# Performance work log

Measured on AMD Instinct MI355X. Metric: run time of the kernel, lower is better.

Reference implementation:

```python
import jax, jax.numpy as jnp
import numpy as np

B, S = 64, 4096
IN_CH, HID, OUT_CH, LIFT, MODES, NLAYERS = 2, 64, 3, 256, 16, 4
FREQ = S // 2 + 1


def setup_inputs() -> dict:
    key = jax.random.key(0)
    ks = jax.random.split(key, 10)
    g = lambda k, shp, s=0.02: (jax.random.normal(k, shp, jnp.float32) * s)
    return {
        "x": jax.random.normal(ks[0], (B, S, IN_CH), jnp.float32),
        "lift_w1": g(ks[1], (LIFT, IN_CH), 0.1),
        "lift_b1": jnp.zeros((LIFT,), jnp.float32),
        "lift_w2": g(ks[2], (HID, LIFT)),
        "lift_b2": jnp.zeros((HID,), jnp.float32),
        # spectral weights per layer: real/imag parts of [in, out, modes]
        "spec_wr": g(ks[3], (NLAYERS, HID, HID, MODES), 1.0 / HID),
        "spec_wi": g(ks[4], (NLAYERS, HID, HID, MODES), 1.0 / HID),
        "skip_w": g(ks[5], (NLAYERS, HID, HID)),
        "skip_b": jnp.zeros((NLAYERS, HID), jnp.float32),
        "proj_w1": g(ks[6], (LIFT, HID)),
        "proj_b1": jnp.zeros((LIFT,), jnp.float32),
        "proj_w2": g(ks[7], (OUT_CH, LIFT)),
        "proj_b2": jnp.zeros((OUT_CH,), jnp.float32),
    }


def _gelu(x):
    return jax.nn.gelu(x, approximate=False)  # torch F.gelu default (exact)


def reference(x, lift_w1, lift_b1, lift_w2, lift_b2, spec_wr, spec_wi,
              skip_w, skip_b, proj_w1, proj_b1, proj_w2, proj_b2):
    # x: (B, S, 2) -> permute to channels-first (B, 2, S), fused into einsum
    h = jnp.einsum('bsi,oi->bos', x, lift_w1) + lift_b1[None, :, None]  # (B, 256, S)
    h = _gelu(h)
    h = jnp.einsum('bcs,oc->bos', h, lift_w2) + lift_b2[None, :, None]  # (B, 64, S)

    for l in range(NLAYERS):
        # spectral conv: rfft -> keep low modes -> complex mix -> irfft
        xf = jnp.fft.rfft(h, axis=-1)[..., :MODES]            # (B, HID, MODES) complex
        w = spec_wr[l] + 1j * spec_wi[l]                       # (HID, HID, MODES)
        yk = jnp.einsum('bim,iom->bom', xf, w)                 # (B, HID, MODES)
        yf = jnp.zeros((h.shape[0], HID, FREQ), jnp.complex64).at[..., :MODES].set(yk)
        spec = jnp.fft.irfft(yf, n=S, axis=-1)                 # (B, HID, S)
        skip = jnp.einsum('bcs,oc->bos', h, skip_w[l]) + skip_b[l][None, :, None]
        h = spec + skip
        if l < NLAYERS - 1:
            h = _gelu(h)

    h = _gelu(jnp.einsum('bcs,oc->bos', h, proj_w1) + proj_b1[None, :, None])
    out_seq = jnp.einsum('bcs,oc->bos', h, proj_w2) + proj_b2[None, :, None]  # (B, 3, S)
    # AdaptiveAvgPool1d(1) + squeeze(-1) == mean over length
    return out_seq.mean(axis=-1)  # (B, 3)
```

## Files before the change

### kernel.cpp

```cpp
#include <hip/hip_runtime.h>
#include <math.h>

#define B_    64
#define S_    4096
#define HID   64
#define LIFT  256
#define MODES 16
#define NL    4

#define OFF_H     0
#define OFF_ETB   16777216
#define OFF_XFY   (OFF_ETB + 131072)
#define OFF_SKH   (OFF_XFY + 131072)
#define OFF_SKL   (OFF_SKH + 8192)
#define OFF_W2HI  (OFF_SKL + 8192)
#define OFF_W2LO  (OFF_W2HI + 8192)
#define OFF_P1HI  (OFF_W2LO + 8192)
#define OFF_P1LO  (OFF_P1HI + 8192)
#define OFF_PART  (OFF_P1LO + 8192)
#define OFF_W1B   (OFF_PART + 12288)

typedef short short8 __attribute__((ext_vector_type(8)));
typedef float f32x4  __attribute__((ext_vector_type(4)));
typedef unsigned uint8v __attribute__((ext_vector_type(8)));
#define MFMA16 __builtin_amdgcn_mfma_f32_16x16x32_bf16

__device__ __forceinline__ float gelu_f(float x) {
  float z = fabsf(x) * 0.70710678118654752440f;
  float p = 1.0f + z * (0.0705230784f + z * (0.0422820123f +
            z * (0.0092705272f + z * (0.0001520143f +
            z * (0.0002765672f + z * 0.0000430638f)))));
  float r = __builtin_amdgcn_rcpf(p);
  r = r * r;
  r = r * r;
  r = r * r;
  r = r * r;
  float q = 0.5f * r;
  float phi = (x >= 0.0f) ? (1.0f - q) : q;
  return x * phi;
}
__device__ __forceinline__ unsigned short f2bf(float x) {
  unsigned u = __float_as_uint(x);
  u += 0x7fffu + ((u >> 16) & 1u);
  return (unsigned short)(u >> 16);
}
__device__ __forceinline__ float bf2f(unsigned short b) {
  return __uint_as_float(((unsigned)b) << 16);
}
__device__ __forceinline__ unsigned packsplit(float x) {
  unsigned short hi = f2bf(x);
  unsigned short lo = f2bf(x - bf2f(hi));
  return (unsigned)hi | ((unsigned)lo << 16);
}
__device__ __forceinline__ void unpk8(const unsigned* pk, short8& h8, short8& l8) {
  #pragma unroll
  for (int j = 0; j < 8; ++j) {
    unsigned u = pk[j];
    h8[j] = (short)(u & 0xffffu);
    l8[j] = (short)(u >> 16);
  }
}

__global__ void k_init(const float* __restrict__ lift_w2,
                       const float* __restrict__ skip_w,
                       const float* __restrict__ proj_w1,
                       const float* __restrict__ lift_w1,
                       const float* __restrict__ lift_b1,
                       float* __restrict__ ws) {
  unsigned* etab = (unsigned*)(ws + OFF_ETB);
  unsigned short* skh = (unsigned short*)(ws + OFF_SKH);
  unsigned short* skl = (unsigned short*)(ws + OFF_SKL);
  unsigned short* w2hi = (unsigned short*)(ws + OFF_W2HI);
  unsigned short* w2lo = (unsigned short*)(ws + OFF_W2LO);
  unsigned short* p1hi = (unsigned short*)(ws + OFF_P1HI);
  unsigned short* p1lo = (unsigned short*)(ws + OFF_P1LO);
  float4* w1b = (float4*)(ws + OFF_W1B);
  int idx = blockIdx.x * 256 + threadIdx.x;
  int stride = gridDim.x * 256;
  for (int k = idx; k < 4096 * 32; k += stride) {
    int s = k >> 5, c = k & 31;
    int m = c & 15;
    int r = (m * s) & 4095;
    float th = (float)(2.0 * 3.14159265358979323846 / 4096.0) * (float)r;
    float sn, cn; sincosf(th, &sn, &cn);
    float v = (c < 16) ? cn : -sn;
    etab[k] = packsplit(v);
  }
  for (int k = idx; k < NL * HID * HID; k += stride) {
    float w = skip_w[k];
    unsigned short hi = f2bf(w);
    skh[k] = hi; skl[k] = f2bf(w - bf2f(hi));
  }
  for (int k = idx; k < HID * LIFT; k += stride) {
    float w = lift_w2[k];
    unsigned short hi = f2bf(w);
    w2hi[k] = hi; w2lo[k] = f2bf(w - bf2f(hi));
  }
  for (int k = idx; k < LIFT * HID; k += stride) {
    float w = proj_w1[k];
    unsigned short hi = f2bf(w);
    p1hi[k] = hi; p1lo[k] = f2bf(w - bf2f(hi));
  }
  for (int k = idx; k < LIFT; k += stride) {
    w1b[k] = make_float4(lift_w1[2 * k], lift_w1[2 * k + 1], lift_b1[k], 0.f);
  }
  for (int k = idx; k < 12288; k += stride)
    ws[OFF_PART + k] = 0.f;
}

__global__ __launch_bounds__(256, 2) void k_lift(
    const float* __restrict__ x, const float4* __restrict__ W1B,
    const float* __restrict__ b2,
    const unsigned short* __restrict__ Whi,
    const unsigned short* __restrict__ Wlo,
    unsigned* __restrict__ Hp) {
  int tid = threadIdx.x;
  int b = blockIdx.y, s0 = blockIdx.x * 256;
  int lane = tid & 63, wv = tid >> 6, quad = lane >> 4, n16 = lane & 15;
  int sw = s0 + wv * 64;
  int cq = quad * 8;
  float2 xv[4];
  #pragma unroll
  for (int nt = 0; nt < 4; ++nt)
    xv[nt] = ((const float2*)x)[b * S_ + sw + nt * 16 + n16];
  f32x4 acc[4][4];
  #pragma unroll
  for (int mt = 0; mt < 4; ++mt)
    #pragma unroll
    for (int nt = 0; nt < 4; ++nt) acc[mt][nt] = (f32x4){0.f, 0.f, 0.f, 0.f};

  #pragma unroll 1
  for (int k = 0; k < 8; ++k) {
    short8 ah[4], al[4];
    #pragma unroll
    for (int mt = 0; mt < 4; ++mt) {
      int aoff = (mt * 16 + n16) * 256 + k * 32 + cq;
      ah[mt] = *(const short8*)(Whi + aoff);
      al[mt] = *(const short8*)(Wlo + aoff);
    }
    float4 w[8];
    #pragma unroll
    for (int j = 0; j < 8; ++j) w[j] = W1B[k * 32 + cq + j];
    #pragma unroll
    for (int nt = 0; nt < 4; ++nt) {
      short8 bh, bl;
      #pragma unroll
      for (int j = 0; j < 8; ++j) {
        float t = gelu_f(w[j].x * xv[nt].x + w[j].y * xv[nt].y + w[j].z);
        unsigned pk = packsplit(t);
        bh[j] = (short)(pk & 0xffffu);
        bl[j] = (short)(pk >> 16);
      }
      #pragma unroll
      for (int mt = 0; mt < 4; ++mt) {
        acc[mt][nt] = MFMA16(ah[mt], bh, acc[mt][nt], 0, 0, 0);
        acc[mt][nt] = MFMA16(ah[mt], bl, acc[mt][nt], 0, 0, 0);
        acc[mt][nt] = MFMA16(al[mt], bh, acc[mt][nt], 0, 0, 0);
      }
    }
  }
  #pragma unroll
  for (int mt = 0; mt < 4; ++mt) {
    int o0 = mt * 16 + quad * 4;
    float4 bb = *(const float4*)&b2[o0];
    #pragma unroll
    for (int nt = 0; nt < 4; ++nt) {
      int sc = sw + nt * 16 + n16;
      unsigned* hp = Hp + ((size_t)b * HID + o0) * S_ + sc;
      hp[0]            = packsplit(acc[mt][nt][0] + bb.x);
      hp[(size_t)S_]   = packsplit(acc[mt][nt][1] + bb.y);
      hp[(size_t)2*S_] = packsplit(acc[mt][nt][2] + bb.z);
      hp[(size_t)3*S_] = packsplit(acc[mt][nt][3] + bb.w);
    }
  }
}

__global__ __launch_bounds__(256, 4) void k_fft_fwd(
    const unsigned* __restrict__ Hp, const unsigned* __restrict__ Etab,
    float* __restrict__ xf) {
  __shared__ float red[4 * 512];
  int tid = threadIdx.x;
  int i0 = blockIdx.x * 16, b = blockIdx.y, ks = blockIdx.z;
  int lane = tid & 63, wv = tid >> 6, quad = lane >> 4, n16 = lane & 15;
  const unsigned* hb = Hp + ((size_t)b * HID + i0 + n16) * S_;
  int g = ks * 4 + wv;
  f32x4 acc0 = (f32x4){0.f,0.f,0.f,0.f}, acc1 = (f32x4){0.f,0.f,0.f,0.f};
  #pragma unroll 1
  for (int kt = 0; kt < 8; ++kt) {
    int sb = g * 256 + kt * 32 + quad * 8;
    uint8v av = *(const uint8v*)(hb + sb);
    short8 ah, al;
    #pragma unroll
    for (int j = 0; j < 8; ++j) {
      unsigned u = av[j];
      ah[j] = (short)(u & 0xffffu); al[j] = (short)(u >> 16);
    }
    unsigned q0[8], q1[8];
    #pragma unroll
    for (int j = 0; j < 8; ++j) {
      q0[j] = Etab[(sb + j) * 32 + n16];
      q1[j] = Etab[(sb + j) * 32 + 16 + n16];
    }
    short8 bh0, bl0, bh1, bl1;
    unpk8(q0, bh0, bl0);
    unpk8(q1, bh1, bl1);
    acc0 = MFMA16(ah, bh0, acc0, 0, 0, 0);
    acc0 = MFMA16(ah, bl0, acc0, 0, 0, 0);
    acc0 = MFMA16(al, bh0, acc0, 0, 0, 0);
    acc1 = MFMA16(ah, bh1, acc1, 0, 0, 0);
    acc1 = MFMA16(ah, bl1, acc1, 0, 0, 0);
    acc1 = MFMA16(al, bh1, acc1, 0, 0, 0);
  }
  #pragma unroll
  for (int r = 0; r < 4; ++r) {
    red[wv * 512 + (quad * 4 + r) * 32 + n16]      = acc0[r];
    red[wv * 512 + (quad * 4 + r) * 32 + 16 + n16] = acc1[r];
  }
  __syncthreads();
  #pragma unroll
  for (int u = 0; u < 2; ++u) {
    int t = u * 256 + tid;
    int il = t >> 5, c = t & 31;
    float v = red[t] + red[512 + t] + red[1024 + t] + red[1536 + t];
    atomicAdd(&xf[(size_t)b * 2048 + (i0 + il) * 32 + c], v);
  }
}

__global__ __launch_bounds__(256) void k_mix(
    const float* __restrict__ wr_, const float* __restrict__ wi_,
    float* __restrict__ xfy) {
  int tid = threadIdx.x;
  int b = blockIdx.x;
  __shared__ float xr[HID * MODES], xi[HID * MODES];
  const float* xfb = xfy + (size_t)b * 2048;
  for (int u = tid; u < HID * MODES; u += 256) {
    int i = u >> 4, m = u & 15;
    xr[u] = xfb[i * 32 + m];
    xi[u] = xfb[i * 32 + 16 + m];
  }
  __syncthreads();
  const float invS = 1.0f / (float)S_;
  unsigned* yk = (unsigned*)xfy + (size_t)b * 2048;
  #pragma unroll
  for (int pp = 0; pp < 4; ++pp) {
    int p = pp * 256 + tid;
    int o = p >> 4, m = p & 15;
    float yr = 0.f, yi = 0.f;
    for (int i2 = 0; i2 < HID; ++i2) {
      float wr = wr_[(i2 * HID + o) * MODES + m];
      float wi = wi_[(i2 * HID + o) * MODES + m];
      float xrv = xr[i2 * MODES + m], xiv = xi[i2 * MODES + m];
      yr += xrv * wr - xiv * wi;
      yi += xrv * wi + xiv * wr;
    }
    float fac = (m == 0) ? invS : 2.f * invS;
    yk[o * 32 + m]      = packsplit(yr * fac);
    yk[o * 32 + 16 + m] = packsplit(yi * fac);
  }
}

template <bool ACT>
__global__ __launch_bounds__(256, 2) void k_spec_skip(
    const unsigned short* __restrict__ Shi,
    const unsigned short* __restrict__ Slo,
    const float* __restrict__ skb,
    const unsigned* __restrict__ Yk,
    const unsigned* __restrict__ Etab,
    unsigned* __restrict__ Hp) {
  int tid = threadIdx.x;
  int s0 = blockIdx.x * 256, b = blockIdx.y;
  int lane = tid & 63, wv = tid >> 6, quad = lane >> 4, n16 = lane & 15;
  int sw = s0 + wv * 64;
  f32x4 acc[4][4];
  #pragma unroll
  for (int mt = 0; mt < 4; ++mt)
    #pragma unroll
    for (int nt = 0; nt < 4; ++nt) acc[mt][nt] = (f32x4){0.f,0.f,0.f,0.f};
  {
    short8 yh[4], yl[4];
    #pragma unroll
    for (int mt = 0; mt < 4; ++mt) {
      uint8v yv = *(const uint8v*)(Yk + (size_t)b * 2048 + (mt * 16 + n16) * 32 + quad * 8);
      #pragma unroll
      for (int j = 0; j < 8; ++j) {
        unsigned u = yv[j];
        yh[mt][j] = (short)(u & 0xffffu); yl[mt][j] = (short)(u >> 16);
      }
    }
    #pragma unroll
    for (int nt = 0; nt < 4; ++nt) {
      int sc = sw + nt * 16 + n16;
      uint8v tv = *(const uint8v*)(Etab + (size_t)sc * 32 + quad * 8);
      short8 th, tl;
      #pragma unroll
      for (int j = 0; j < 8; ++j) {
        unsigned u = tv[j];
        th[j] = (short)(u & 0xffffu); tl[j] = (short)(u >> 16);
      }
      #pragma unroll
      for (int mt = 0; mt < 4; ++mt) {
        acc[mt][nt] = MFMA16(yh[mt], th, acc[mt][nt], 0, 0, 0);
        acc[mt][nt] = MFMA16(yh[mt], tl, acc[mt][nt], 0, 0, 0);
        acc[mt][nt] = MFMA16(yl[mt], th, acc[mt][nt], 0, 0, 0);
      }
    }
  }
  const unsigned* hb = Hp + (size_t)b * HID * S_;
  #pragma unroll
  for (int kk = 0; kk < 2; ++kk) {
    short8 skh[4], skl[4];
    #pragma unroll
    for (int mt = 0; mt < 4; ++mt) {
      int off = (mt * 16 + n16) * 64 + kk * 32 + quad * 8;
      skh[mt] = *(const short8*)(Shi + off);
      skl[mt] = *(const short8*)(Slo + off);
    }
    #pragma unroll
    for (int nt = 0; nt < 4; ++nt) {
      int sc = sw + nt * 16 + n16;
      unsigned pk[8];
      #pragma unroll
      for (int j = 0; j < 8; ++j)
        pk[j] = hb[(size_t)(kk * 32 + quad * 8 + j) * S_ + sc];
      short8 bh, bl;
      unpk8(pk, bh, bl);
      #pragma unroll
      for (int mt = 0; mt < 4; ++mt) {
        acc[mt][nt] = MFMA16(skh[mt], bh, acc[mt][nt], 0, 0, 0);
        acc[mt][nt] = MFMA16(skh[mt], bl, acc[mt][nt], 0, 0, 0);
        acc[mt][nt] = MFMA16(skl[mt], bh, acc[mt][nt], 0, 0, 0);
      }
    }
  }
  #pragma unroll
  for (int mt = 0; mt < 4; ++mt) {
    int o0 = mt * 16 + quad * 4;
    float4 bb = *(const float4*)&skb[o0];
    #pragma unroll
    for (int nt = 0; nt < 4; ++nt) {
      int sc = sw + nt * 16 + n16;
      #pragma unroll
      for (int r = 0; r < 4; ++r) {
        float v = acc[mt][nt][r] + ((const float*)&bb)[r];
        if (ACT) v = gelu_f(v);
        Hp[(size_t)(b * HID + o0 + r) * S_ + sc] = packsplit(v);
      }
    }
  }
}

__global__ __launch_bounds__(256, 2) void k_proj(
    const unsigned short* __restrict__ Phi,
    const unsigned short* __restrict__ Plo,
    const float* __restrict__ pb1, const float* __restrict__ pw2,
    const unsigned* __restrict__ Hp, float* __restrict__ part) {
  __shared__ unsigned Bp[64 * 65];
  __shared__ float red[12];
  int tid = threadIdx.x;
  int s0 = blockIdx.x * 64, b = blockIdx.y;
  int lane = tid & 63, wv = tid >> 6, quad = lane >> 4, n16 = lane & 15;
  #pragma unroll
  for (int u = 0; u < 16; ++u) {
    int idx = u * 256 + tid;
    int c = idx >> 6, s = idx & 63;
    Bp[c * 65 + s] = Hp[((size_t)b * HID + c) * S_ + s0 + s];
  }
  __syncthreads();
  int m0 = blockIdx.z * 128 + wv * 32;
  f32x4 acc[2][4];
  #pragma unroll
  for (int mt = 0; mt < 2; ++mt)
    #pragma unroll
    for (int nt = 0; nt < 4; ++nt) acc[mt][nt] = (f32x4){0.f,0.f,0.f,0.f};
  #pragma unroll
  for (int kk = 0; kk < 2; ++kk) {
    int kbase = kk * 32 + quad * 8;
    short8 ah[2], al[2];
    #pragma unroll
    for (int mt = 0; mt < 2; ++mt) {
      int aoff = (m0 + mt * 16 + n16) * 64 + kbase;
      ah[mt] = *(const short8*)(Phi + aoff);
      al[mt] = *(const short8*)(Plo + aoff);
    }
    #pragma unroll
    for (int nt = 0; nt < 4; ++nt) {
      int sc = nt * 16 + n16;
      unsigned pk[8];
      #pragma unroll
      for (int j = 0; j < 8; ++j) pk[j] = Bp[(kbase + j) * 65 + sc];
      short8 bh, bl;
      unpk8(pk, bh, bl);
      #pragma unroll
      for (int mt = 0; mt < 2; ++mt) {
        acc[mt][nt] = MFMA16(ah[mt], bh, acc[mt][nt], 0, 0, 0);
        acc[mt][nt] = MFMA16(ah[mt], bl, acc[mt][nt], 0, 0, 0);
        acc[mt][nt] = MFMA16(al[mt], bh, acc[mt][nt], 0, 0, 0);
      }
    }
  }
  float o0 = 0.f, o1 = 0.f, o2 = 0.f;
  #pragma unroll
  for (int mt = 0; mt < 2; ++mt) {
    int c2b = m0 + mt * 16 + quad * 4;
    float4 bb = *(const float4*)&pb1[c2b];
    float4 p0 = *(const float4*)&pw2[c2b];
    float4 p1 = *(const float4*)&pw2[256 + c2b];
    float4 p2 = *(const float4*)&pw2[512 + c2b];
    #pragma unroll
    for (int nt = 0; nt < 4; ++nt) {
      f32x4 a = acc[mt][nt];
      float t0 = gelu_f(a[0] + bb.x);
      float t1 = gelu_f(a[1] + bb.y);
      float t2 = gelu_f(a[2] + bb.z);
      float t3 = gelu_f(a[3] + bb.w);
      o0 += p0.x * t0 + p0.y * t1 + p0.z * t2 + p0.w * t3;
      o1 += p1.x * t0 + p1.y * t1 + p1.z * t2 + p1.w * t3;
      o2 += p2.x * t0 + p2.y * t1 + p2.z * t2 + p2.w * t3;
    }
  }
  #pragma unroll
  for (int off = 32; off > 0; off >>= 1) {
    o0 += __shfl_xor(o0, off, 64);
    o1 += __shfl_xor(o1, off, 64);
    o2 += __shfl_xor(o2, off, 64);
  }
  if (lane == 0) { red[wv*3+0] = o0; red[wv*3+1] = o1; red[wv*3+2] = o2; }
  __syncthreads();
  if (tid < 3) {
    float sum = red[tid] + red[3 + tid] + red[6 + tid] + red[9 + tid];
    atomicAdd(&part[(b * 64 + blockIdx.x) * 3 + tid], sum);
  }
}

__global__ void k_final(const float* __restrict__ part,
                        const float* __restrict__ pb2,
                        float* __restrict__ out) {
  int t = threadIdx.x;
  if (t < B_ * 3) {
    int b = t / 3, j = t % 3;
    float s = 0.f;
    for (int k = 0; k < 64; ++k) s += part[(b * 64 + k) * 3 + j];
    out[t] = s * (1.0f / (float)S_) + pb2[j];
  }
}

extern "C" void kernel_launch(void* const* d_in, const int* in_sizes, int n_in,
                              void* d_out, int out_size, void* d_ws, size_t ws_size,
                              hipStream_t stream) {
  const float* x   = (const float*)d_in[0];
  const float* lw1 = (const float*)d_in[1];
  const float* lb1 = (const float*)d_in[2];
  const float* lw2 = (const float*)d_in[3];
  const float* lb2 = (const float*)d_in[4];
  const float* swr = (const float*)d_in[5];
  const float* swi = (const float*)d_in[6];
  const float* skw = (const float*)d_in[7];
  const float* skb = (const float*)d_in[8];
  const float* pw1 = (const float*)d_in[9];
  const float* pb1 = (const float*)d_in[10];
  const float* pw2 = (const float*)d_in[11];
  const float* pb2 = (const float*)d_in[12];
  float* ws = (float*)d_ws;
  unsigned* Hp  = (unsigned*)(ws + OFF_H);
  unsigned* ETB = (unsigned*)(ws + OFF_ETB);
  float*    XFY = ws + OFF_XFY;

  k_init<<<256, 256, 0, stream>>>(lw2, skw, pw1, lw1, lb1, ws);
  k_lift<<<dim3(S_ / 256, B_), 256, 0, stream>>>(
      x, (const float4*)(ws + OFF_W1B), lb2,
      (const unsigned short*)(ws + OFF_W2HI),
      (const unsigned short*)(ws + OFF_W2LO), Hp);
  for (int l = 0; l < NL; ++l) {
    hipMemsetAsync(XFY, 0, (size_t)B_ * 2048 * sizeof(float), stream);
    k_fft_fwd<<<dim3(4, B_, 4), 256, 0, stream>>>(Hp, ETB, XFY);
    k_mix<<<B_, 256, 0, stream>>>(swr + l * HID * HID * MODES,
                                  swi + l * HID * HID * MODES, XFY);
    if (l < NL - 1)
      k_spec_skip<true><<<dim3(S_ / 256, B_), 256, 0, stream>>>(
          (const unsigned short*)(ws + OFF_SKH) + l * HID * HID,
          (const unsigned short*)(ws + OFF_SKL) + l * HID * HID,
          skb + l * HID, (const unsigned*)XFY, ETB, Hp);
    else
      k_spec_skip<false><<<dim3(S_ / 256, B_), 256, 0, stream>>>(
          (const unsigned short*)(ws + OFF_SKH) + l * HID * HID,
          (const unsigned short*)(ws + OFF_SKL) + l * HID * HID,
          skb + l * HID, (const unsigned*)XFY, ETB, Hp);
  }
  k_proj<<<dim3(S_ / 64, B_, 2), 256, 0, stream>>>(
      (const unsigned short*)(ws + OFF_P1HI),
      (const unsigned short*)(ws + OFF_P1LO),
      pb1, pw2, Hp, ws + OFF_PART);
  k_final<<<1, 256, 0, stream>>>(ws + OFF_PART, pb2, (float*)d_out);
}
```

Baseline: 526.6 us.

## Transpose twiddle table and software-pipeline loads in lift and spectral-skip kernels

The DFT twiddle table moves to a mode-major layout, so the forward FFT kernel reads each lane's twiddles as contiguous 8-word vectors instead of strided scalar gathers, while the inverse path now does strided scalar reads. The lift kernel double-buffers its weight loads across k iterations so memory fetches overlap the GELU and MFMA work. The spectral/skip kernel issues the skip-input and weight loads before the inverse-DFT MFMAs, giving memory latency something to hide behind. The cost is higher register pressure, which may spill or reduce occupancy.

```diff
diff --git a/kernel.cpp b/kernel.cpp
--- a/kernel.cpp
+++ b/kernel.cpp
@@ -51,6 +51,11 @@
   unsigned short hi = f2bf(x);
   unsigned short lo = f2bf(x - bf2f(hi));
   return (unsigned)hi | ((unsigned)lo << 16);
+}
+__device__ __forceinline__ void split2(float x, short& hi, short& lo) {
+  unsigned short h = f2bf(x);
+  hi = (short)h;
+  lo = (short)f2bf(x - bf2f(h));
 }
 __device__ __forceinline__ void unpk8(const unsigned* pk, short8& h8, short8& l8) {
   #pragma unroll
@@ -77,8 +82,8 @@
   float4* w1b = (float4*)(ws + OFF_W1B);
   int idx = blockIdx.x * 256 + threadIdx.x;
   int stride = gridDim.x * 256;
-  for (int k = idx; k < 4096 * 32; k += stride) {
-    int s = k >> 5, c = k & 31;
+  for (int k = idx; k < 32 * 4096; k += stride) {
+    int c = k >> 12, s = k & 4095;
     int m = c & 15;
     int r = (m * s) & 4095;
     float th = (float)(2.0 * 3.14159265358979323846 / 4096.0) * (float)r;
@@ -106,6 +111,44 @@
   }
   for (int k = idx; k < 12288; k += stride)
     ws[OFF_PART + k] = 0.f;
+}
+
+__device__ __forceinline__ void lift_load(
+    int k, int n16, int cq,
+    const unsigned short* __restrict__ Whi,
+    const unsigned short* __restrict__ Wlo,
+    const float4* __restrict__ W1B,
+    short8 ah[4], short8 al[4], float4 w[8]) {
+  #pragma unroll
+  for (int mt = 0; mt < 4; ++mt) {
+    int aoff = (mt * 16 + n16) * 256 + k * 32 + cq;
+    ah[mt] = *(const short8*)(Whi + aoff);
+    al[mt] = *(const short8*)(Wlo + aoff);
+  }
+  #pragma unroll
+  for (int j = 0; j < 8; ++j) w[j] = W1B[k * 32 + cq + j];
+}
+
+__device__ __forceinline__ void lift_step(
+    const short8 ah[4], const short8 al[4], const float4 w[8],
+    const float2 xv[4], f32x4 acc[4][4]) {
+  #pragma unroll
+  for (int nt = 0; nt < 4; ++nt) {
+    short8 bh, bl;
+    #pragma unroll
+    for (int j = 0; j < 8; ++j) {
+      float t = gelu_f(w[j].x * xv[nt].x + w[j].y * xv[nt].y + w[j].z);
+      short hv, lv;
+      split2(t, hv, lv);
+      bh[j] = hv; bl[j] = lv;
+    }
+    #pragma unroll
+    for (int mt = 0; mt < 4; ++mt) {
+      acc[mt][nt] = MFMA16(ah[mt], bh, acc[mt][nt], 0, 0, 0);
+      acc[mt][nt] = MFMA16(ah[mt], bl, acc[mt][nt], 0, 0, 0);
+      acc[mt][nt] = MFMA16(al[mt], bh, acc[mt][nt], 0, 0, 0);
+    }
+  }
 }
 
 __global__ __launch_bounds__(256, 2) void k_lift(
@@ -129,36 +172,18 @@
     #pragma unroll
     for (int nt = 0; nt < 4; ++nt) acc[mt][nt] = (f32x4){0.f, 0.f, 0.f, 0.f};
 
+  short8 ahA[4], alA[4], ahB[4], alB[4];
+  float4 wA[8], wB[8];
+  lift_load(0, n16, cq, Whi, Wlo, W1B, ahA, alA, wA);
   #pragma unroll 1
-  for (int k = 0; k < 8; ++k) {
-    short8 ah[4], al[4];
-    #pragma unroll
-    for (int mt = 0; mt < 4; ++mt) {
-      int aoff = (mt * 16 + n16) * 256 + k * 32 + cq;
-      ah[mt] = *(const short8*)(Whi + aoff);
-      al[mt] = *(const short8*)(Wlo + aoff);
-    }
-    float4 w[8];
-    #pragma unroll
-    for (int j = 0; j < 8; ++j) w[j] = W1B[k * 32 + cq + j];
-    #pragma unroll
-    for (int nt = 0; nt < 4; ++nt) {
-      short8 bh, bl;
-      #pragma unroll
-      for (int j = 0; j < 8; ++j) {
-        float t = gelu_f(w[j].x * xv[nt].x + w[j].y * xv[nt].y + w[j].z);
-        unsigned pk = packsplit(t);
-        bh[j] = (short)(pk & 0xffffu);
-        bl[j] = (short)(pk >> 16);
-      }
-      #pragma unroll
-      for (int mt = 0; mt < 4; ++mt) {
-        acc[mt][nt] = MFMA16(ah[mt], bh, acc[mt][nt], 0, 0, 0);
-        acc[mt][nt] = MFMA16(ah[mt], bl, acc[mt][nt], 0, 0, 0);
-        acc[mt][nt] = MFMA16(al[mt], bh, acc[mt][nt], 0, 0, 0);
-      }
-    }
-  }
+  for (int k2 = 0; k2 < 4; ++k2) {
+    lift_load(2 * k2 + 1, n16, cq, Whi, Wlo, W1B, ahB, alB, wB);
+    lift_step(ahA, alA, wA, xv, acc);
+    if (k2 < 3)
+      lift_load(2 * k2 + 2, n16, cq, Whi, Wlo, W1B, ahA, alA, wA);
+    lift_step(ahB, alB, wB, xv, acc);
+  }
+
   #pragma unroll
   for (int mt = 0; mt < 4; ++mt) {
     int o0 = mt * 16 + quad * 4;
@@ -176,34 +201,33 @@
 }
 
 __global__ __launch_bounds__(256, 4) void k_fft_fwd(
-    const unsigned* __restrict__ Hp, const unsigned* __restrict__ Etab,
+    const unsigned* __restrict__ Hp, const unsigned* __restrict__ EtabT,
     float* __restrict__ xf) {
   __shared__ float red[4 * 512];
   int tid = threadIdx.x;
   int i0 = blockIdx.x * 16, b = blockIdx.y, ks = blockIdx.z;
   int lane = tid & 63, wv = tid >> 6, quad = lane >> 4, n16 = lane & 15;
   const unsigned* hb = Hp + ((size_t)b * HID + i0 + n16) * S_;
+  const unsigned* e0 = EtabT + (size_t)n16 * 4096;
+  const unsigned* e1 = EtabT + (size_t)(16 + n16) * 4096;
   int g = ks * 4 + wv;
   f32x4 acc0 = (f32x4){0.f,0.f,0.f,0.f}, acc1 = (f32x4){0.f,0.f,0.f,0.f};
   #pragma unroll 1
   for (int kt = 0; kt < 8; ++kt) {
     int sb = g * 256 + kt * 32 + quad * 8;
     uint8v av = *(const uint8v*)(hb + sb);
-    short8 ah, al;
+    uint8v q0v = *(const uint8v*)(e0 + sb);
+    uint8v q1v = *(const uint8v*)(e1 + sb);
+    short8 ah, al, bh0, bl0, bh1, bl1;
     #pragma unroll
     for (int j = 0; j < 8; ++j) {
       unsigned u = av[j];
       ah[j] = (short)(u & 0xffffu); al[j] = (short)(u >> 16);
-    }
-    unsigned q0[8], q1[8];
-    #pragma unroll
-    for (int j = 0; j < 8; ++j) {
-      q0[j] = Etab[(sb + j) * 32 + n16];
-      q1[j] = Etab[(sb + j) * 32 + 16 + n16];
-    }
-    short8 bh0, bl0, bh1, bl1;
-    unpk8(q0, bh0, bl0);
-    unpk8(q1, bh1, bl1);
+      unsigned u0 = q0v[j];
+      bh0[j] = (short)(u0 & 0xffffu); bl0[j] = (short)(u0 >> 16);
+      unsigned u1 = q1v[j];
+      bh1[j] = (short)(u1 & 0xffffu); bl1[j] = (short)(u1 >> 16);
+    }
     acc0 = MFMA16(ah, bh0, acc0, 0, 0, 0);
     acc0 = MFMA16(ah, bl0, acc0, 0, 0, 0);
     acc0 = MFMA16(al, bh0, acc0, 0, 0, 0);
@@ -265,17 +289,35 @@
     const unsigned short* __restrict__ Slo,
     const float* __restrict__ skb,
     const unsigned* __restrict__ Yk,
-    const unsigned* __restrict__ Etab,
+    const unsigned* __restrict__ EtabT,
     unsigned* __restrict__ Hp) {
   int tid = threadIdx.x;
   int s0 = blockIdx.x * 256, b = blockIdx.y;
   int lane = tid & 63, wv = tid >> 6, quad = lane >> 4, n16 = lane & 15;
   int sw = s0 + wv * 64;
+  const unsigned* hb = Hp + (size_t)b * HID * S_;
   f32x4 acc[4][4];
   #pragma unroll
   for (int mt = 0; mt < 4; ++mt)
     #pragma unroll
     for (int nt = 0; nt < 4; ++nt) acc[mt][nt] = (f32x4){0.f,0.f,0.f,0.f};
+
+  unsigned pk0[4][8];
+  #pragma unroll
+  for (int nt = 0; nt < 4; ++nt) {
+    int sc = sw + nt * 16 + n16;
+    #pragma unroll
+    for (int j = 0; j < 8; ++j)
+      pk0[nt][j] = hb[(size_t)(quad * 8 + j) * S_ + sc];
+  }
+  short8 sk0h[4], sk0l[4];
+  #pragma unroll
+  for (int mt = 0; mt < 4; ++mt) {
+    int off = (mt * 16 + n16) * 64 + quad * 8;
+    sk0h[mt] = *(const short8*)(Shi + off);
+    sk0l[mt] = *(const short8*)(Slo + off);
+  }
+
   {
     short8 yh[4], yl[4];
     #pragma unroll
@@ -290,13 +332,12 @@
     #pragma unroll
     for (int nt = 0; nt < 4; ++nt) {
       int sc = sw + nt * 16 + n16;
-      uint8v tv = *(const uint8v*)(Etab + (size_t)sc * 32 + quad * 8);
+      unsigned tvj[8];
+      #pragma unroll
+      for (int j = 0; j < 8; ++j)
+        tvj[j] = EtabT[(size_t)(quad * 8 + j) * 4096 + sc];
       short8 th, tl;
-      #pragma unroll
-      for (int j = 0; j < 8; ++j) {
-        unsigned u = tv[j];
-        th[j] = (short)(u & 0xffffu); tl[j] = (short)(u >> 16);
-      }
+      unpk8(tvj, th, tl);
       #pragma unroll
       for (int mt = 0; mt < 4; ++mt) {
         acc[mt][nt] = MFMA16(yh[mt], th, acc[mt][nt], 0, 0, 0);
@@ -305,33 +346,45 @@
       }
     }
   }
-  const unsigned* hb = Hp + (size_t)b * HID * S_;
-  #pragma unroll
-  for (int kk = 0; kk < 2; ++kk) {
-    short8 skh[4], skl[4];
+
+  unsigned pk1[4][8];
+  #pragma unroll
+  for (int nt = 0; nt < 4; ++nt) {
+    int sc = sw + nt * 16 + n16;
+    #pragma unroll
+    for (int j = 0; j < 8; ++j)
+      pk1[nt][j] = hb[(size_t)(32 + quad * 8 + j) * S_ + sc];
+  }
+  short8 sk1h[4], sk1l[4];
+  #pragma unroll
+  for (int mt = 0; mt < 4; ++mt) {
+    int off = (mt * 16 + n16) * 64 + 32 + quad * 8;
+    sk1h[mt] = *(const short8*)(Shi + off);
+    sk1l[mt] = *(const short8*)(Slo + off);
+  }
+  #pragma unroll
+  for (int nt = 0; nt < 4; ++nt) {
+    short8 bh, bl;
+    unpk8(pk0[nt], bh, bl);
     #pragma unroll
     for (int mt = 0; mt < 4; ++mt) {
-      int off = (mt * 16 + n16) * 64 + kk * 32 + quad * 8;
-      skh[mt] = *(const short8*)(Shi + off);
-      skl[mt] = *(const short8*)(Slo + off);
-    }
-    #pragma unroll
-    for (int nt = 0; nt < 4; ++nt) {
-      int sc = sw + nt * 16 + n16;
-      unsigned pk[8];
-      #pragma unroll
-      for (int j = 0; j < 8; ++j)
-        pk[j] = hb[(size_t)(kk * 32 + quad * 8 + j) * S_ + sc];
-      short8 bh, bl;
-      unpk8(pk, bh, bl);
-      #pragma unroll
-      for (int mt = 0; mt < 4; ++mt) {
-        acc[mt][nt] = MFMA16(skh[mt], bh, acc[mt][nt], 0, 0, 0);
-        acc[mt][nt] = MFMA16(skh[mt], bl, acc[mt][nt], 0, 0, 0);
-        acc[mt][nt] = MFMA16(skl[mt], bh, acc[mt][nt], 0, 0, 0);
-      }
-    }
-  }
+      acc[mt][nt] = MFMA16(sk0h[mt], bh, acc[mt][nt], 0, 0, 0);
+      acc[mt][nt] = MFMA16(sk0h[mt], bl, acc[mt][nt], 0, 0, 0);
+      acc[mt][nt] = MFMA16(sk0l[mt], bh, acc[mt][nt], 0, 0, 0);
+    }
+  }
+  #pragma unroll
+  for (int nt = 0; nt < 4; ++nt) {
+    short8 bh, bl;
+    unpk8(pk1[nt], bh, bl);
+    #pragma unroll
+    for (int mt = 0; mt < 4; ++mt) {
+      acc[mt][nt] = MFMA16(sk1h[mt], bh, acc[mt][nt], 0, 0, 0);
+      acc[mt][nt] = MFMA16(sk1h[mt], bl, acc[mt][nt], 0, 0, 0);
+      acc[mt][nt] = MFMA16(sk1l[mt], bh, acc[mt][nt], 0, 0, 0);
+    }
+  }
+
   #pragma unroll
   for (int mt = 0; mt < 4; ++mt) {
     int o0 = mt * 16 + quad * 4;
```

New measurement: 556.3 us. 1.06x slower.
